# Kernel tuning notes

Measured on AMD Instinct MI355X. Metric: run time of the kernel, lower is better.

Reference implementation:

```python
import jax, jax.numpy as jnp
import numpy as np

EPS = 1e-7
LAMBDA_COORD = 10.0
LAMBDA_NOOBJ = 0.5
LAMBDA_OBJ = 1.0


def setup_inputs() -> dict:
    key = jax.random.key(0)
    k1, k2, k3, k4 = jax.random.split(key, 4)
    B, A, C, G = 64, 3, 20, 76
    predictions = jax.random.normal(k1, (B, A * (5 + C), G, G), dtype=jnp.float32) * 0.5
    txy = jax.random.uniform(k2, (B, A, G, G, 2), dtype=jnp.float32)
    twh = jax.random.normal(k3, (B, A, G, G, 2), dtype=jnp.float32) * 0.3
    tconf = (jax.random.uniform(k4, (B, A, G, G, 1), dtype=jnp.float32) < 0.05).astype(jnp.float32)
    targets = jnp.concatenate([txy, twh, tconf], axis=-1)
    anchors = jnp.array([[1.25, 1.625], [2.0, 3.75], [4.125, 2.875]], dtype=jnp.float32)
    return {"predictions": predictions, "targets": targets, "anchors": anchors}


def _bce(p, t):
    # elementwise binary cross-entropy; p in (0,1) from sigmoid
    return -(t * jnp.log(p) + (1.0 - t) * jnp.log1p(-p))


def _ciou_loss_elem(pb, tb):
    # pb, tb: [..., 4] corner boxes; returns elementwise (1 - ciou)
    x1p, y1p, x2p, y2p = pb[..., 0], pb[..., 1], pb[..., 2], pb[..., 3]
    x1t, y1t, x2t, y2t = tb[..., 0], tb[..., 1], tb[..., 2], tb[..., 3]
    iw = jnp.clip(jnp.minimum(x2p, x2t) - jnp.maximum(x1p, x1t), 0.0)
    ih = jnp.clip(jnp.minimum(y2p, y2t) - jnp.maximum(y1p, y1t), 0.0)
    inter = iw * ih
    area_p = jnp.clip(x2p - x1p, 0.0) * jnp.clip(y2p - y1p, 0.0)
    area_t = jnp.clip(x2t - x1t, 0.0) * jnp.clip(y2t - y1t, 0.0)
    union = area_p + area_t - inter + EPS
    iou = inter / union
    rho2 = ((x1p + x2p - x1t - x2t) * 0.5) ** 2 + ((y1p + y2p - y1t - y2t) * 0.5) ** 2
    en_w = jnp.clip(jnp.maximum(x2p, x2t) - jnp.minimum(x1p, x1t), EPS)
    en_h = jnp.clip(jnp.maximum(y2p, y2t) - jnp.minimum(y1p, y1t), EPS)
    c2 = en_w ** 2 + en_h ** 2
    w_p = jnp.clip(x2p - x1p, EPS); h_p = jnp.clip(y2p - y1p, EPS)
    w_t = jnp.clip(x2t - x1t, EPS); h_t = jnp.clip(y2t - y1t, EPS)
    v = (4.0 / (jnp.pi ** 2)) * (jnp.arctan(w_t / h_t) - jnp.arctan(w_p / h_p)) ** 2
    alpha = jax.lax.stop_gradient(v / (1.0 - iou + v + EPS))
    ciou = iou - rho2 / (c2 + EPS) - alpha * v
    return 1.0 - ciou


def reference(predictions, targets, anchors):
    B, Ch, G, _ = predictions.shape
    A = anchors.shape[0]
    C = Ch // A - 5
    p = predictions.reshape(B, A, 5 + C, G, G).transpose(0, 1, 3, 4, 2)  # [B,A,G,G,5+C]
    pred_xy = jax.nn.sigmoid(p[..., :2])
    pred_wh = p[..., 2:4]
    pred_conf = jax.nn.sigmoid(p[..., 4])
    pred_cls = jax.nn.sigmoid(p[..., 5:])
    obj = targets[..., 4] > 0          # [B,A,G,G]
    n_obj = jnp.sum(obj.astype(jnp.float32))
    n_noobj = jnp.sum((~obj).astype(jnp.float32))
    gy, gx = jnp.meshgrid(jnp.arange(G, dtype=jnp.float32), jnp.arange(G, dtype=jnp.float32), indexing='ij')
    inv_g = 1.0 / G
    aw = anchors[:, 0][None, :, None, None] * inv_g
    ah = anchors[:, 1][None, :, None, None] * inv_g
    # predicted corner boxes
    pcx = (gx + pred_xy[..., 0]) * inv_g
    pcy = (gy + pred_xy[..., 1]) * inv_g
    pw = jnp.exp(pred_wh[..., 0]) * aw
    ph = jnp.exp(pred_wh[..., 1]) * ah
    pred_corners = jnp.clip(jnp.stack([pcx - pw / 2, pcy - ph / 2, pcx + pw / 2, pcy + ph / 2], axis=-1), 0.0, 1.0)
    # target corner boxes
    tcx = (gx + targets[..., 0]) * inv_g
    tcy = (gy + targets[..., 1]) * inv_g
    tw = jnp.exp(targets[..., 2]) * aw
    th = jnp.exp(targets[..., 3]) * ah
    tgt_corners = jnp.clip(jnp.stack([tcx - tw / 2, tcy - th / 2, tcx + tw / 2, tcy + th / 2], axis=-1), 0.0, 1.0)
    ciou_l = _ciou_loss_elem(pred_corners, tgt_corners)  # [B,A,G,G]
    coord_sum = jnp.sum(jnp.where(obj, ciou_l, 0.0))
    coord_loss = jnp.where(n_obj > 0, coord_sum / jnp.maximum(n_obj, 1.0), 0.0)
    conf_bce = _bce(pred_conf, targets[..., 4])
    obj_loss = jnp.where(n_obj > 0, jnp.sum(jnp.where(obj, conf_bce, 0.0)) / jnp.maximum(n_obj, 1.0), 0.0)
    noobj_bce = -jnp.log1p(-pred_conf)  # BCE with target 0
    noobj_loss = jnp.where(n_noobj > 0, jnp.sum(jnp.where(~obj, noobj_bce, 0.0)) / jnp.maximum(n_noobj, 1.0), 0.0)
    if C > 0:
        cls_bce = -jnp.log(pred_cls)  # BCE with target 1
        cls_sum = jnp.sum(jnp.where(obj[..., None], cls_bce, 0.0))
        class_loss = jnp.where(n_obj > 0, cls_sum / jnp.maximum(n_obj * C, 1.0), 0.0)
    else:
        class_loss = jnp.float32(0.0)
    total = LAMBDA_COORD * coord_loss + LAMBDA_OBJ * obj_loss + LAMBDA_NOOBJ * noobj_loss + class_loss
    return total
```

## Files before the change

kernel.cpp:

```cpp
#include <hip/hip_runtime.h>
#include <math.h>

namespace {

constexpr int   kBd    = 64;
constexpr int   kA     = 3;
constexpr int   kC     = 20;
constexpr int   kG     = 76;
constexpr int   kGG    = kG * kG;
constexpr int   kCH    = 5 + kC;
constexpr int   kNCell = kBd * kA * kGG;
constexpr int   kNC4   = kNCell / 4;
constexpr int   kBlk   = 256;
constexpr int   kGrid  = kNC4 / kBlk;
constexpr int   kCellsPerBlk = kBlk * 4;
constexpr float kEps   = 1e-7f;
constexpr float kInvG  = 1.0f / (float)kG;
constexpr float kPiO2  = 1.57079632679f;

constexpr int kPartStride = 8;

__device__ __forceinline__ float softplus_fast(float x) {
  return fmaxf(x, 0.0f) + __logf(1.0f + __expf(-fabsf(x)));
}
__device__ __forceinline__ float sigmoidf(float x) {
  return 1.0f / (1.0f + __expf(-x));
}
__device__ __forceinline__ float clamp01(float x) {
  return fminf(fmaxf(x, 0.0f), 1.0f);
}

__device__ __forceinline__ float atan_ratio(float num, float den) {
  const float z  = __fdividef(fminf(num, den), fmaxf(num, den));
  const float z2 = z * z;
  float p = 0.0208351f;
  p = fmaf(p, z2, -0.0851330f);
  p = fmaf(p, z2,  0.1801410f);
  p = fmaf(p, z2, -0.3302995f);
  p = fmaf(p, z2,  0.9998660f);
  const float a = z * p;
  return (num > den) ? (kPiO2 - a) : a;
}

__device__ __forceinline__ float ciou_cell(
    int cell, float tx, float ty, float tw, float th,
    const float* __restrict__ preds, const float* __restrict__ anchors) {
  const int ba = cell / kGG;
  const int j  = cell - ba * kGG;
  const int a  = ba % kA;
  const int gy = j / kG;
  const int gx = j - gy * kG;
  const float fgx = (float)gx, fgy = (float)gy;

  const float aw = anchors[2 * a]     * kInvG;
  const float ah = anchors[2 * a + 1] * kInvG;

  const float* pb = preds + (size_t)ba * kCH * kGG + j;
  const float px  = pb[0];
  const float py  = pb[(size_t)1 * kGG];
  const float pwv = pb[(size_t)2 * kGG];
  const float phv = pb[(size_t)3 * kGG];

  const float pcx = (fgx + sigmoidf(px)) * kInvG;
  const float pcy = (fgy + sigmoidf(py)) * kInvG;
  const float pw  = __expf(pwv) * aw;
  const float ph  = __expf(phv) * ah;
  const float x1p = clamp01(pcx - 0.5f * pw);
  const float y1p = clamp01(pcy - 0.5f * ph);
  const float x2p = clamp01(pcx + 0.5f * pw);
  const float y2p = clamp01(pcy + 0.5f * ph);

  const float tcx = (fgx + tx) * kInvG;
  const float tcy = (fgy + ty) * kInvG;
  const float twv = __expf(tw) * aw;
  const float thv = __expf(th) * ah;
  const float x1t = clamp01(tcx - 0.5f * twv);
  const float y1t = clamp01(tcy - 0.5f * thv);
  const float x2t = clamp01(tcx + 0.5f * twv);
  const float y2t = clamp01(tcy + 0.5f * thv);

  const float iw     = fmaxf(fminf(x2p, x2t) - fmaxf(x1p, x1t), 0.0f);
  const float ih     = fmaxf(fminf(y2p, y2t) - fmaxf(y1p, y1t), 0.0f);
  const float inter  = iw * ih;
  const float area_p = fmaxf(x2p - x1p, 0.0f) * fmaxf(y2p - y1p, 0.0f);
  const float area_t = fmaxf(x2t - x1t, 0.0f) * fmaxf(y2t - y1t, 0.0f);
  const float uni    = area_p + area_t - inter + kEps;
  const float iou    = __fdividef(inter, uni);
  const float dx     = (x1p + x2p - x1t - x2t) * 0.5f;
  const float dy     = (y1p + y2p - y1t - y2t) * 0.5f;
  const float rho2   = dx * dx + dy * dy;
  const float enw    = fmaxf(fmaxf(x2p, x2t) - fminf(x1p, x1t), kEps);
  const float enh    = fmaxf(fmaxf(y2p, y2t) - fminf(y1p, y1t), kEps);
  const float c2     = enw * enw + enh * enh;
  const float wp     = fmaxf(x2p - x1p, kEps);
  const float hp     = fmaxf(y2p - y1p, kEps);
  const float wt     = fmaxf(x2t - x1t, kEps);
  const float ht     = fmaxf(y2t - y1t, kEps);
  const float k4pi2  = 4.0f / (float)(M_PI * M_PI);
  const float dat    = atan_ratio(wt, ht) - atan_ratio(wp, hp);
  const float v      = k4pi2 * dat * dat;
  const float alpha  = __fdividef(v, 1.0f - iou + v + kEps);
  const float ciou   = iou - __fdividef(rho2, c2 + kEps) - alpha * v;
  return 1.0f - ciou;
}

template <int N, int BLK>
__device__ __forceinline__ void block_reduceN(float r[N], float* out) {
  #pragma unroll
  for (int off = 32; off > 0; off >>= 1) {
    #pragma unroll
    for (int s = 0; s < N; ++s) r[s] += __shfl_down(r[s], off, 64);
  }
  __shared__ float red[BLK / 64][N];
  const int lane = threadIdx.x & 63;
  const int wid  = threadIdx.x >> 6;
  if (lane == 0) {
    #pragma unroll
    for (int s = 0; s < N; ++s) red[wid][s] = r[s];
  }
  __syncthreads();
  if (threadIdx.x == 0) {
    #pragma unroll
    for (int s = 0; s < N; ++s) {
      float a = red[0][s];
      #pragma unroll
      for (int w = 1; w < BLK / 64; ++w) a += red[w][s];
      out[s] = a;
    }
  }
}

__global__ __launch_bounds__(kBlk) void yolo_fused(
    const float* __restrict__ preds,
    const float* __restrict__ tgts,
    const float* __restrict__ anchors,
    float* __restrict__ part) {
  __shared__ int    s_list[kCellsPerBlk];
  __shared__ float4 s_tgt[kCellsPerBlk];
  __shared__ int    s_wtot[kBlk / 64];

  const int b    = blockIdx.x;
  const int q    = b * kBlk + threadIdx.x;
  const int cell = q * 4;
  const int ba   = cell / kGG;
  const int j0   = cell - ba * kGG;

  union { float4 v[5]; float f[20]; } T;
  const float4* tb = (const float4*)(tgts + (size_t)cell * 5);
  #pragma unroll
  for (int i = 0; i < 5; ++i) T.v[i] = tb[i];

  const float* p4p = preds + (size_t)ba * kCH * kGG + (size_t)4 * kGG + j0;
  const float4 P4 = *(const float4*)p4p;
  const float p4a[4] = { P4.x, P4.y, P4.z, P4.w };

  float r[5] = {0.f, 0.f, 0.f, 0.f, 0.f};
  unsigned msk = 0u;

  #pragma unroll
  for (int i = 0; i < 4; ++i) {
    const bool obj = T.f[i * 5 + 4] > 0.0f;
    const float sp = softplus_fast(p4a[i]);
    if (obj) {
      r[0] += sp - p4a[i];
      r[4] += 1.0f;
      msk |= (1u << i);
    } else {
      r[1] += sp;
    }
  }
  const int cnt = __popc(msk);

  const int lane = threadIdx.x & 63;
  const int wid  = threadIdx.x >> 6;
  int incl = cnt;
  #pragma unroll
  for (int off = 1; off < 64; off <<= 1) {
    const int n = __shfl_up(incl, off, 64);
    if (lane >= off) incl += n;
  }
  const int excl = incl - cnt;

  if (lane == 63) s_wtot[wid] = incl;
  __syncthreads();

  int wbase = 0;
  #pragma unroll
  for (int w = 0; w < kBlk / 64; ++w) wbase += (w < wid) ? s_wtot[w] : 0;
  const int total = s_wtot[0] + s_wtot[1] + s_wtot[2] + s_wtot[3];

  int p = wbase + excl;
  #pragma unroll
  for (int i = 0; i < 4; ++i) {
    if ((msk >> i) & 1u) {
      s_list[p] = cell + i;
      s_tgt[p]  = make_float4(T.f[i * 5 + 0], T.f[i * 5 + 1],
                              T.f[i * 5 + 2], T.f[i * 5 + 3]);
      ++p;
    }
  }
  __syncthreads();

  for (int i = threadIdx.x; i < total; i += kBlk) {
    const float4 t4 = s_tgt[i];
    r[2] += ciou_cell(s_list[i], t4.x, t4.y, t4.z, t4.w, preds, anchors);
  }
  const int nwork = total * 4;
  for (int w = threadIdx.x; w < nwork; w += kBlk) {
    const int i = w >> 2;
    const int t = w & 3;
    const int c   = s_list[i];
    const int cba = c / kGG;
    const int cj  = c - cba * kGG;
    const float* cp = preds + (size_t)cba * kCH * kGG + (size_t)(5 + 5 * t) * kGG + cj;
    float cacc = 0.0f;
    #pragma unroll
    for (int k = 0; k < 5; ++k) cacc += softplus_fast(-cp[(size_t)k * kGG]);
    r[3] += cacc;
  }

  block_reduceN<5, kBlk>(r, part + (size_t)b * kPartStride);
}

__global__ __launch_bounds__(256) void yolo_finish(
    const float* __restrict__ part, float* __restrict__ out) {
  float r[5] = {0.f, 0.f, 0.f, 0.f, 0.f};
  for (int i = threadIdx.x; i < kGrid; i += 256) {
    const float* pi = part + (size_t)i * kPartStride;
    #pragma unroll
    for (int s = 0; s < 5; ++s) r[s] += pi[s];
  }
  __shared__ float outbuf[5];
  block_reduceN<5, 256>(r, outbuf);
  __syncthreads();
  if (threadIdx.x == 0) {
    const float objc    = outbuf[0];
    const float noobj   = outbuf[1];
    const float coord   = outbuf[2];
    const float cls     = outbuf[3];
    const float n_obj   = outbuf[4];
    const float n_noobj = (float)kNCell - n_obj;

    const float coord_loss = (n_obj > 0.f)   ? coord / fmaxf(n_obj, 1.f)   : 0.f;
    const float obj_loss   = (n_obj > 0.f)   ? objc  / fmaxf(n_obj, 1.f)   : 0.f;
    const float noobj_loss = (n_noobj > 0.f) ? noobj / fmaxf(n_noobj, 1.f) : 0.f;
    const float class_loss = (n_obj > 0.f)   ? cls / fmaxf(n_obj * (float)kC, 1.f) : 0.f;

    out[0] = 10.0f * coord_loss + 1.0f * obj_loss + 0.5f * noobj_loss + class_loss;
  }
}

}

extern "C" void kernel_launch(void* const* d_in, const int* in_sizes, int n_in,
                              void* d_out, int out_size, void* d_ws, size_t ws_size,
                              hipStream_t stream) {
  const float* preds   = (const float*)d_in[0];
  const float* tgts    = (const float*)d_in[1];
  const float* anchors = (const float*)d_in[2];
  float* out  = (float*)d_out;
  float* part = (float*)d_ws;

  yolo_fused<<<kGrid, kBlk, 0, stream>>>(preds, tgts, anchors, part);
  yolo_finish<<<1, 256, 0, stream>>>(part, out);
}
```

Measured before the change: 26.93 us.

## Gather class logits per 16-cell group with float4 loads instead of per-cell scalars

Builds a per-block bitmask of object cells in groups of 16 and compacts the groups that hold any object. Class-logit loads then become one float4 per channel per 4 cells inside each active group, masked by the nibble, instead of scattered scalar loads per object cell. The aim is coalesced, wider memory transactions for the class term. In exchange it loads and processes some non-object cells and adds a shared-memory atomic plus a ballot compaction step with an extra barrier.

```diff
diff --git a/kernel.cpp b/kernel.cpp
--- a/kernel.cpp
+++ b/kernel.cpp
@@ -14,6 +14,7 @@
 constexpr int   kBlk   = 256;
 constexpr int   kGrid  = kNC4 / kBlk;
 constexpr int   kCellsPerBlk = kBlk * 4;
+constexpr int   kGrpPerBlk   = kCellsPerBlk / 16;
 constexpr float kEps   = 1e-7f;
 constexpr float kInvG  = 1.0f / (float)kG;
 constexpr float kPiO2  = 1.57079632679f;
@@ -138,12 +139,16 @@
   __shared__ int    s_list[kCellsPerBlk];
   __shared__ float4 s_tgt[kCellsPerBlk];
   __shared__ int    s_wtot[kBlk / 64];
-
-  const int b    = blockIdx.x;
-  const int q    = b * kBlk + threadIdx.x;
-  const int cell = q * 4;
-  const int ba   = cell / kGG;
-  const int j0   = cell - ba * kGG;
+  __shared__ int    s_gmask[kGrpPerBlk];
+  __shared__ int    s_glist[kGrpPerBlk];
+  __shared__ int    s_ngrp;
+
+  const int b     = blockIdx.x;
+  const int tid   = threadIdx.x;
+  const int base  = b * kCellsPerBlk;
+  const int cell  = base + tid * 4;
+  const int ba    = cell / kGG;
+  const int j0    = cell - ba * kGG;
 
   union { float4 v[5]; float f[20]; } T;
   const float4* tb = (const float4*)(tgts + (size_t)cell * 5);
@@ -171,8 +176,8 @@
   }
   const int cnt = __popc(msk);
 
-  const int lane = threadIdx.x & 63;
-  const int wid  = threadIdx.x >> 6;
+  const int lane = tid & 63;
+  const int wid  = tid >> 6;
   int incl = cnt;
   #pragma unroll
   for (int off = 1; off < 64; off <<= 1) {
@@ -182,6 +187,7 @@
   const int excl = incl - cnt;
 
   if (lane == 63) s_wtot[wid] = incl;
+  if (tid < kGrpPerBlk) s_gmask[tid] = 0;
   __syncthreads();
 
   int wbase = 0;
@@ -189,6 +195,7 @@
   for (int w = 0; w < kBlk / 64; ++w) wbase += (w < wid) ? s_wtot[w] : 0;
   const int total = s_wtot[0] + s_wtot[1] + s_wtot[2] + s_wtot[3];
 
+  if (msk) atomicOr(&s_gmask[tid >> 2], (int)(msk << ((tid & 3) * 4)));
   int p = wbase + excl;
   #pragma unroll
   for (int i = 0; i < 4; ++i) {
@@ -201,21 +208,42 @@
   }
   __syncthreads();
 
-  for (int i = threadIdx.x; i < total; i += kBlk) {
+  if (wid == 0) {
+    const bool has = s_gmask[lane] != 0;
+    const unsigned long long bal = __ballot(has);
+    if (has) {
+      const int pos = __popcll(bal & ((1ULL << lane) - 1ULL));
+      s_glist[pos] = lane;
+    }
+    if (lane == 0) s_ngrp = __popcll(bal);
+  }
+  __syncthreads();
+
+  for (int i = tid; i < total; i += kBlk) {
     const float4 t4 = s_tgt[i];
     r[2] += ciou_cell(s_list[i], t4.x, t4.y, t4.z, t4.w, preds, anchors);
   }
-  const int nwork = total * 4;
-  for (int w = threadIdx.x; w < nwork; w += kBlk) {
-    const int i = w >> 2;
-    const int t = w & 3;
-    const int c   = s_list[i];
-    const int cba = c / kGG;
-    const int cj  = c - cba * kGG;
-    const float* cp = preds + (size_t)cba * kCH * kGG + (size_t)(5 + 5 * t) * kGG + cj;
+
+  const int ngrp   = s_ngrp;
+  const int nitems = ngrp * (kC * 4);
+  for (int w = tid; w < nitems; w += kBlk) {
+    const int gi  = w / 80;
+    const int rem = w - gi * 80;
+    const int ch  = rem >> 2;
+    const int qtr = rem & 3;
+    const int g   = s_glist[gi];
+    const unsigned m16 = (unsigned)s_gmask[g];
+    const int nib  = (m16 >> (qtr * 4)) & 0xF;
+    const int c0   = base + g * 16 + qtr * 4;
+    const int cba  = c0 / kGG;
+    const int cj   = c0 - cba * kGG;
+    const float4 v = *(const float4*)(preds + (size_t)cba * kCH * kGG +
+                                      (size_t)(5 + ch) * kGG + cj);
     float cacc = 0.0f;
-    #pragma unroll
-    for (int k = 0; k < 5; ++k) cacc += softplus_fast(-cp[(size_t)k * kGG]);
+    cacc += (nib & 1) ? softplus_fast(-v.x) : 0.0f;
+    cacc += (nib & 2) ? softplus_fast(-v.y) : 0.0f;
+    cacc += (nib & 4) ? softplus_fast(-v.z) : 0.0f;
+    cacc += (nib & 8) ? softplus_fast(-v.w) : 0.0f;
     r[3] += cacc;
   }
 
```

Result: slower. 28.82 us (+7.0%).

## Replace block-level compaction of object cells with per-thread dense processing

Applied to the files above, without the earlier changes.

Removes the shared-memory prefix-sum compaction of object cells and its two barriers. Each thread now handles CIoU and class BCE for its own four cells directly, using float4 loads of box and class channels when any of its cells has an object. This drops the scan, the shared writes and the scattered gathers, but with about 5% positives many threads in a wave will have one positive. Those waves then load all 24 extra channels per thread, so memory traffic and divergence go up.

```diff
diff --git a/kernel.cpp b/kernel.cpp
--- a/kernel.cpp
+++ b/kernel.cpp
@@ -13,7 +13,6 @@
 constexpr int   kNC4   = kNCell / 4;
 constexpr int   kBlk   = 256;
 constexpr int   kGrid  = kNC4 / kBlk;
-constexpr int   kCellsPerBlk = kBlk * 4;
 constexpr float kEps   = 1e-7f;
 constexpr float kInvG  = 1.0f / (float)kG;
 constexpr float kPiO2  = 1.57079632679f;
@@ -42,25 +41,10 @@
   return (num > den) ? (kPiO2 - a) : a;
 }
 
-__device__ __forceinline__ float ciou_cell(
-    int cell, float tx, float ty, float tw, float th,
-    const float* __restrict__ preds, const float* __restrict__ anchors) {
-  const int ba = cell / kGG;
-  const int j  = cell - ba * kGG;
-  const int a  = ba % kA;
-  const int gy = j / kG;
-  const int gx = j - gy * kG;
-  const float fgx = (float)gx, fgy = (float)gy;
-
-  const float aw = anchors[2 * a]     * kInvG;
-  const float ah = anchors[2 * a + 1] * kInvG;
-
-  const float* pb = preds + (size_t)ba * kCH * kGG + j;
-  const float px  = pb[0];
-  const float py  = pb[(size_t)1 * kGG];
-  const float pwv = pb[(size_t)2 * kGG];
-  const float phv = pb[(size_t)3 * kGG];
-
+__device__ __forceinline__ float ciou_vals(
+    float px, float py, float pwv, float phv,
+    float tx, float ty, float tw, float th,
+    float fgx, float fgy, float aw, float ah) {
   const float pcx = (fgx + sigmoidf(px)) * kInvG;
   const float pcy = (fgy + sigmoidf(py)) * kInvG;
   const float pw  = __expf(pwv) * aw;
@@ -130,15 +114,11 @@
   }
 }
 
-__global__ __launch_bounds__(kBlk) void yolo_fused(
+__global__ __launch_bounds__(kBlk) void yolo_dense(
     const float* __restrict__ preds,
     const float* __restrict__ tgts,
     const float* __restrict__ anchors,
     float* __restrict__ part) {
-  __shared__ int    s_list[kCellsPerBlk];
-  __shared__ float4 s_tgt[kCellsPerBlk];
-  __shared__ int    s_wtot[kBlk / 64];
-
   const int b    = blockIdx.x;
   const int q    = b * kBlk + threadIdx.x;
   const int cell = q * 4;
@@ -150,8 +130,9 @@
   #pragma unroll
   for (int i = 0; i < 5; ++i) T.v[i] = tb[i];
 
-  const float* p4p = preds + (size_t)ba * kCH * kGG + (size_t)4 * kGG + j0;
-  const float4 P4 = *(const float4*)p4p;
+  const float* pb = preds + (size_t)ba * kCH * kGG + j0;
+
+  const float4 P4 = *(const float4*)(pb + (size_t)4 * kGG);
   const float p4a[4] = { P4.x, P4.y, P4.z, P4.w };
 
   float r[5] = {0.f, 0.f, 0.f, 0.f, 0.f};
@@ -169,54 +150,44 @@
       r[1] += sp;
     }
   }
-  const int cnt = __popc(msk);
-
-  const int lane = threadIdx.x & 63;
-  const int wid  = threadIdx.x >> 6;
-  int incl = cnt;
-  #pragma unroll
-  for (int off = 1; off < 64; off <<= 1) {
-    const int n = __shfl_up(incl, off, 64);
-    if (lane >= off) incl += n;
-  }
-  const int excl = incl - cnt;
-
-  if (lane == 63) s_wtot[wid] = incl;
-  __syncthreads();
-
-  int wbase = 0;
-  #pragma unroll
-  for (int w = 0; w < kBlk / 64; ++w) wbase += (w < wid) ? s_wtot[w] : 0;
-  const int total = s_wtot[0] + s_wtot[1] + s_wtot[2] + s_wtot[3];
-
-  int p = wbase + excl;
-  #pragma unroll
-  for (int i = 0; i < 4; ++i) {
-    if ((msk >> i) & 1u) {
-      s_list[p] = cell + i;
-      s_tgt[p]  = make_float4(T.f[i * 5 + 0], T.f[i * 5 + 1],
-                              T.f[i * 5 + 2], T.f[i * 5 + 3]);
-      ++p;
-    }
-  }
-  __syncthreads();
-
-  for (int i = threadIdx.x; i < total; i += kBlk) {
-    const float4 t4 = s_tgt[i];
-    r[2] += ciou_cell(s_list[i], t4.x, t4.y, t4.z, t4.w, preds, anchors);
-  }
-  const int nwork = total * 4;
-  for (int w = threadIdx.x; w < nwork; w += kBlk) {
-    const int i = w >> 2;
-    const int t = w & 3;
-    const int c   = s_list[i];
-    const int cba = c / kGG;
-    const int cj  = c - cba * kGG;
-    const float* cp = preds + (size_t)cba * kCH * kGG + (size_t)(5 + 5 * t) * kGG + cj;
+
+  if (msk) {
+    const int a = ba % kA;
+    const float aw = anchors[2 * a]     * kInvG;
+    const float ah = anchors[2 * a + 1] * kInvG;
+
+    const float4 B0 = *(const float4*)(pb + (size_t)0 * kGG);
+    const float4 B1 = *(const float4*)(pb + (size_t)1 * kGG);
+    const float4 B2 = *(const float4*)(pb + (size_t)2 * kGG);
+    const float4 B3 = *(const float4*)(pb + (size_t)3 * kGG);
+    const float b0a[4] = {B0.x, B0.y, B0.z, B0.w};
+    const float b1a[4] = {B1.x, B1.y, B1.z, B1.w};
+    const float b2a[4] = {B2.x, B2.y, B2.z, B2.w};
+    const float b3a[4] = {B3.x, B3.y, B3.z, B3.w};
+
+    #pragma unroll
+    for (int i = 0; i < 4; ++i) {
+      if ((msk >> i) & 1u) {
+        const int j  = j0 + i;
+        const int gy = j / kG;
+        const int gx = j - gy * kG;
+        r[2] += ciou_vals(b0a[i], b1a[i], b2a[i], b3a[i],
+                          T.f[i * 5 + 0], T.f[i * 5 + 1],
+                          T.f[i * 5 + 2], T.f[i * 5 + 3],
+                          (float)gx, (float)gy, aw, ah);
+      }
+    }
+
     float cacc = 0.0f;
     #pragma unroll
-    for (int k = 0; k < 5; ++k) cacc += softplus_fast(-cp[(size_t)k * kGG]);
-    r[3] += cacc;
+    for (int c = 0; c < kC; ++c) {
+      const float4 v = *(const float4*)(pb + (size_t)(5 + c) * kGG);
+      cacc += (msk & 1u) ? softplus_fast(-v.x) : 0.0f;
+      cacc += (msk & 2u) ? softplus_fast(-v.y) : 0.0f;
+      cacc += (msk & 4u) ? softplus_fast(-v.z) : 0.0f;
+      cacc += (msk & 8u) ? softplus_fast(-v.w) : 0.0f;
+    }
+    r[3] = cacc;
   }
 
   block_reduceN<5, kBlk>(r, part + (size_t)b * kPartStride);
@@ -261,6 +232,6 @@
   float* out  = (float*)d_out;
   float* part = (float*)d_ws;
 
-  yolo_fused<<<kGrid, kBlk, 0, stream>>>(preds, tgts, anchors, part);
+  yolo_dense<<<kGrid, kBlk, 0, stream>>>(preds, tgts, anchors, part);
   yolo_finish<<<1, 256, 0, stream>>>(part, out);
 }
```

Result: slower. 39.81 us (+47.8%).
